# Performance work log

Measured on AMD Instinct MI355X. Metric: run time of the kernel, lower is better.

The kernel has to match this reference:

```python
import jax, jax.numpy as jnp
import numpy as np

STATE_SIZE = 29
ACTION_SIZE = 3


def setup_inputs() -> dict:
    key = jax.random.key(0)
    ks = jax.random.split(key, 12)

    def row_norm(k, shape, scale=1.0):
        w = jax.random.normal(k, shape, dtype=jnp.float32)
        return w * (scale / jnp.sqrt(jnp.sum(w * w, axis=1, keepdims=True)))

    lrelu_gain = float(np.sqrt(2.0 / (1.0 + 0.01 ** 2)))  # torch calculate_gain('leaky_relu')
    inp = {
        "x": jax.random.normal(ks[0], (1, STATE_SIZE), dtype=jnp.float32),
        "hx": jnp.zeros((1, 128), jnp.float32),
        "cx": jnp.zeros((1, 128), jnp.float32),
        "w1": row_norm(ks[1], (256, STATE_SIZE)) * lrelu_gain,
        "b1": jnp.zeros((256,), jnp.float32),
        "w2": row_norm(ks[2], (256, 256)) * lrelu_gain,
        "b2": jnp.zeros((256,), jnp.float32),
        "w3": row_norm(ks[3], (128, 256)) * lrelu_gain,
        "b3": jnp.zeros((128,), jnp.float32),
        "w4": row_norm(ks[4], (128, 128)) * lrelu_gain,
        "b4": jnp.zeros((128,), jnp.float32),
        "w_ih": jax.random.normal(ks[5], (512, 128), dtype=jnp.float32) * 0.08,
        "b_ih": jnp.zeros((512,), jnp.float32),
        "w_hh": jax.random.normal(ks[6], (512, 128), dtype=jnp.float32) * 0.08,
        "b_hh": jnp.zeros((512,), jnp.float32),
        "w_critic": row_norm(ks[7], (1, 128), 1.0),
        "b_critic": jnp.zeros((1,), jnp.float32),
        "w_actor": row_norm(ks[8], (ACTION_SIZE, 128), 0.01),
        "b_actor": jnp.zeros((ACTION_SIZE,), jnp.float32),
        "w_actor2": row_norm(ks[9], (ACTION_SIZE, 128), 0.01),
        "b_actor2": jnp.zeros((ACTION_SIZE,), jnp.float32),
    }
    return inp


def _lrelu(v):
    return jnp.where(v > 0, v, 0.1 * v)


def reference(x, hx, cx, w1, b1, w2, b2, w3, b3, w4, b4,
              w_ih, b_ih, w_hh, b_hh,
              w_critic, b_critic, w_actor, b_actor, w_actor2, b_actor2):
    h = _lrelu(x @ w1.T + b1)
    h = _lrelu(h @ w2.T + b2)
    h = _lrelu(h @ w3.T + b3)
    h = _lrelu(h @ w4.T + b4)            # [1,128]
    # LSTMCell: gate order i, f, g, o (PyTorch convention)
    gates = h @ w_ih.T + b_ih + hx @ w_hh.T + b_hh  # [1,512]
    i, f, g, o = jnp.split(gates, 4, axis=-1)
    c_new = jax.nn.sigmoid(f) * cx + jax.nn.sigmoid(i) * jnp.tanh(g)
    h_new = jax.nn.sigmoid(o) * jnp.tanh(c_new)      # [1,128]
    value = jnp.squeeze(h_new @ w_critic.T + b_critic)          # scalar
    actor = jax.nn.soft_sign(h_new @ w_actor.T + b_actor)
    actor = jnp.squeeze(actor)                                   # [action_size]
    actor2 = jnp.squeeze(h_new @ w_actor2.T + b_actor2)         # [action_size]
    return (value, actor, actor2)
```

## Files before the change

kernel.cpp:

```cpp
#include <hip/hip_runtime.h>
#include <math.h>


#define NB   61
#define TPB  256
#define MAGIC 0x3A3C5A17u

#define H1_OFF 0
#define H2_OFF 256
#define H3_OFF 512
#define PT_OFF 640

__device__ __forceinline__ float lrelu(float v) { return v > 0.f ? v : 0.1f * v; }
__device__ __forceinline__ float sigm(float v)  { return 1.f / (1.f + __expf(-v)); }
__device__ __forceinline__ float dot4(float4 a, float4 b) {
    return a.x * b.x + a.y * b.y + a.z * b.z + a.w * b.w;
}

__device__ __forceinline__ void send(unsigned long long* p, float v) {
    unsigned lo = __float_as_uint(v);
    unsigned long long pk = (unsigned long long)lo |
                            ((unsigned long long)(lo ^ MAGIC) << 32);
    __hip_atomic_store(p, pk, __ATOMIC_RELAXED, __HIP_MEMORY_SCOPE_AGENT);
}
__device__ __forceinline__ float recv(unsigned long long* p) {
    unsigned long long pk =
        __hip_atomic_load(p, __ATOMIC_RELAXED, __HIP_MEMORY_SCOPE_AGENT);
    unsigned lo = (unsigned)pk, hi = (unsigned)(pk >> 32);
    if ((lo ^ MAGIC) == hi) return __uint_as_float(lo);
    __builtin_amdgcn_s_sleep(2);
    for (;;) {
        pk = __hip_atomic_load(p, __ATOMIC_RELAXED, __HIP_MEMORY_SCOPE_AGENT);
        lo = (unsigned)pk; hi = (unsigned)(pk >> 32);
        if ((lo ^ MAGIC) == hi) return __uint_as_float(lo);
        __builtin_amdgcn_s_sleep(8);
    }
}
__device__ __forceinline__ void touch(unsigned long long* p) {
    unsigned long long v =
        __hip_atomic_load(p, __ATOMIC_RELAXED, __HIP_MEMORY_SCOPE_AGENT);
    asm volatile("" :: "v"(v));
}

__global__ __launch_bounds__(TPB, 1) void a3c_fwd(
    const float* __restrict__ x, const float* __restrict__ hx, const float* __restrict__ cx,
    const float* __restrict__ w1, const float* __restrict__ b1,
    const float* __restrict__ w2, const float* __restrict__ b2,
    const float* __restrict__ w3, const float* __restrict__ b3,
    const float* __restrict__ w4, const float* __restrict__ b4,
    const float* __restrict__ w_ih, const float* __restrict__ b_ih,
    const float* __restrict__ w_hh, const float* __restrict__ b_hh,
    const float* __restrict__ w_critic, const float* __restrict__ b_critic,
    const float* __restrict__ w_actor, const float* __restrict__ b_actor,
    const float* __restrict__ w_actor2, const float* __restrict__ b_actor2,
    float* __restrict__ out, unsigned long long* __restrict__ wsp)
{
    const int blk = blockIdx.x, tid = threadIdx.x;

    if (blk < 32) {
        const int g  = blk;
        const int gc = g * 4;
        const int r  = tid >> 4, p = tid & 15;
        const int gate = r >> 2, cell = r & 3;
        const int grow = gate * 128 + gc + cell;
        const int r4 = tid >> 1, p4 = tid & 1;

        if (tid < 8)       touch(wsp + H3_OFF + tid * 16);
        else if (tid == 8) touch(wsp + PT_OFF + g * 8);

        __shared__ __align__(16) float hx_s[128];
        __shared__ __align__(16) float h3_s[128];
        __shared__ __align__(16) float h4_s[128];
        __shared__ __align__(16) float g_s[16];
        __shared__ __align__(16) float hn_s[4];
        __shared__ __align__(16) float hw_s[28];
        __shared__ __align__(16) float hb_s[8];

        float4 ah0, ah1;
        {
            const float4* wp = (const float4*)(w_hh + grow * 128 + p * 8);
            ah0 = wp[0]; ah1 = wp[1];
        }
        float4 a4[16];
        {
            const float4* wp = (const float4*)(w4 + r4 * 128 + p4 * 64);
            #pragma unroll
            for (int j = 0; j < 16; ++j) a4[j] = wp[j];
        }
        float4 ai0, ai1;
        {
            const float4* wp = (const float4*)(w_ih + grow * 128 + p * 8);
            ai0 = wp[0]; ai1 = wp[1];
        }
        const float bsum = b_ih[grow] + b_hh[grow];
        const float bb4  = b4[r4];
        float cxv = (tid < 4) ? cx[gc + tid] : 0.f;

        if (tid < 128) hx_s[tid] = hx[tid];
        if (tid < 28) {
            int o = tid >> 2, c = tid & 3;
            float v;
            if (o == 0)      v = w_critic[gc + c];
            else if (o < 4)  v = w_actor [(o - 1) * 128 + gc + c];
            else             v = w_actor2[(o - 4) * 128 + gc + c];
            hw_s[tid] = v;
        }
        if (g == 0 && tid == 0) {
            hb_s[0] = b_critic[0];
            hb_s[1] = b_actor[0];  hb_s[2] = b_actor[1];  hb_s[3] = b_actor[2];
            hb_s[4] = b_actor2[0]; hb_s[5] = b_actor2[1]; hb_s[6] = b_actor2[2];
        }
        __syncthreads();

        float g0;
        {
            const float4* hp = (const float4*)(hx_s + p * 8);
            float s = dot4(ah0, hp[0]) + dot4(ah1, hp[1]);
            s += __shfl_xor(s, 1); s += __shfl_xor(s, 2);
            s += __shfl_xor(s, 4); s += __shfl_xor(s, 8);
            g0 = s + bsum;
        }

        if (tid < 128) h3_s[tid] = recv(wsp + H3_OFF + tid);
        __syncthreads();

        {
            const float4* hp = (const float4*)(h3_s + p4 * 64);
            float s = 0.f;
            #pragma unroll
            for (int j = 0; j < 16; ++j) s += dot4(a4[j], hp[j]);
            s += __shfl_xor(s, 1);
            if (p4 == 0) h4_s[r4] = lrelu(s + bb4);
        }
        __syncthreads();

        {
            const float4* hp = (const float4*)(h4_s + p * 8);
            float s = dot4(ai0, hp[0]) + dot4(ai1, hp[1]);
            s += __shfl_xor(s, 1); s += __shfl_xor(s, 2);
            s += __shfl_xor(s, 4); s += __shfl_xor(s, 8);
            if (p == 0) g_s[r] = g0 + s;
        }
        __syncthreads();

        if (tid < 4) {
            float ig = g_s[tid];
            float fg = g_s[4 + tid];
            float gg = g_s[8 + tid];
            float og = g_s[12 + tid];
            float c  = sigm(fg) * cxv + sigm(ig) * tanhf(gg);
            hn_s[tid] = sigm(og) * tanhf(c);
        }
        __syncthreads();

        if (tid < 7) {
            const float* wc = hw_s + tid * 4;
            float s = wc[0] * hn_s[0] + wc[1] * hn_s[1]
                    + wc[2] * hn_s[2] + wc[3] * hn_s[3];
            if (g == 0) s += hb_s[tid];
            send(wsp + PT_OFF + g * 8 + tid, s);
        }
        return;
    }

    if (blk < 36) {
        const int row = (blk - 32) * 64 + (tid >> 2), sub = tid & 3;
        if (tid < 4) touch(wsp + H1_OFF + (blk - 32) * 64 + tid * 16);

        float a[8];
        #pragma unroll
        for (int j = 0; j < 8; ++j) {
            int c = sub * 8 + j;
            a[j] = (c < 29) ? w1[row * 29 + c] : 0.f;
        }
        const float bb1 = b1[row];

        __shared__ __align__(16) float x_s[32];
        if (tid < 32) x_s[tid] = (tid < 29) ? x[tid] : 0.f;
        __syncthreads();

        const float* xp = x_s + sub * 8;
        float s = 0.f;
        #pragma unroll
        for (int j = 0; j < 8; ++j) s += a[j] * xp[j];
        s += __shfl_xor(s, 1); s += __shfl_xor(s, 2);
        if (sub == 0) send(wsp + H1_OFF + row, lrelu(s + bb1));
        return;
    }

    if (blk < 52) {
        const int b = blk - 36;
        const int row = b * 16 + (tid >> 4), p = tid & 15;
        if (tid < 16)       touch(wsp + H1_OFF + tid * 16);
        else if (tid == 16) touch(wsp + H2_OFF + b * 16);

        float4 a2[4];
        {
            const float4* wp = (const float4*)(w2 + row * 256 + p * 16);
            #pragma unroll
            for (int j = 0; j < 4; ++j) a2[j] = wp[j];
        }
        const float bb2 = b2[row];

        __shared__ __align__(16) float h1_s[256];
        h1_s[tid] = recv(wsp + H1_OFF + tid);
        __syncthreads();

        const float4* hp = (const float4*)(h1_s + p * 16);
        float s = 0.f;
        #pragma unroll
        for (int j = 0; j < 4; ++j) s += dot4(a2[j], hp[j]);
        s += __shfl_xor(s, 1); s += __shfl_xor(s, 2);
        s += __shfl_xor(s, 4); s += __shfl_xor(s, 8);
        if (p == 0) send(wsp + H2_OFF + row, lrelu(s + bb2));
        return;
    }

    if (blk < 60) {
        const int b = blk - 52;
        const int row = b * 16 + (tid >> 4), p = tid & 15;
        if (tid < 16)       touch(wsp + H2_OFF + tid * 16);
        else if (tid == 16) touch(wsp + H3_OFF + b * 16);

        float4 a3[4];
        {
            const float4* wp = (const float4*)(w3 + row * 256 + p * 16);
            #pragma unroll
            for (int j = 0; j < 4; ++j) a3[j] = wp[j];
        }
        const float bb3 = b3[row];

        __shared__ __align__(16) float h2_s[256];
        h2_s[tid] = recv(wsp + H2_OFF + tid);
        __syncthreads();

        const float4* hp = (const float4*)(h2_s + p * 16);
        float s = 0.f;
        #pragma unroll
        for (int j = 0; j < 4; ++j) s += dot4(a3[j], hp[j]);
        s += __shfl_xor(s, 1); s += __shfl_xor(s, 2);
        s += __shfl_xor(s, 4); s += __shfl_xor(s, 8);
        if (p == 0) send(wsp + H3_OFF + row, lrelu(s + bb3));
        return;
    }

    {
        if (tid < 32) touch(wsp + PT_OFF + tid * 8);
        __shared__ __align__(16) float ps[224];
        const int g = tid >> 3, h = tid & 7;
        if (h < 7) ps[h * 32 + g] = recv(wsp + PT_OFF + g * 8 + h);
        __syncthreads();
        if (tid < 7) {
            const float* row = ps + tid * 32;
            float s = 0.f;
            #pragma unroll
            for (int j = 0; j < 32; ++j) s += row[j];
            if (tid >= 1 && tid <= 3) s = s / (1.f + fabsf(s));
            out[tid] = s;
        }
    }
}

extern "C" void kernel_launch(void* const* d_in, const int* in_sizes, int n_in,
                              void* d_out, int out_size, void* d_ws, size_t ws_size,
                              hipStream_t stream) {
    const float* x        = (const float*)d_in[0];
    const float* hx       = (const float*)d_in[1];
    const float* cx       = (const float*)d_in[2];
    const float* w1       = (const float*)d_in[3];
    const float* b1       = (const float*)d_in[4];
    const float* w2       = (const float*)d_in[5];
    const float* b2       = (const float*)d_in[6];
    const float* w3       = (const float*)d_in[7];
    const float* b3       = (const float*)d_in[8];
    const float* w4       = (const float*)d_in[9];
    const float* b4       = (const float*)d_in[10];
    const float* w_ih     = (const float*)d_in[11];
    const float* b_ih     = (const float*)d_in[12];
    const float* w_hh     = (const float*)d_in[13];
    const float* b_hh     = (const float*)d_in[14];
    const float* w_critic = (const float*)d_in[15];
    const float* b_critic = (const float*)d_in[16];
    const float* w_actor  = (const float*)d_in[17];
    const float* b_actor  = (const float*)d_in[18];
    const float* w_actor2 = (const float*)d_in[19];
    const float* b_actor2 = (const float*)d_in[20];
    float* out = (float*)d_out;
    unsigned long long* wsp = (unsigned long long*)d_ws;

    a3c_fwd<<<NB, TPB, 0, stream>>>(x, hx, cx, w1, b1, w2, b2, w3, b3, w4, b4,
                                    w_ih, b_ih, w_hh, b_hh,
                                    w_critic, b_critic, w_actor, b_actor,
                                    w_actor2, b_actor2, out, wsp);
}
```

Baseline: 103.0 us.

## Re-partition fused MLP+LSTM stages across 41 blocks with fewer cross-block handoffs

Layer 1 is now computed redundantly inside each layer-2 block, which removes the separate layer-1 stage and its global handoff. Layer 4 moves out of the LSTM blocks into its own 4-block stage. The LSTM gate work shrinks to 16 blocks of 8 cells each, and the final reduction sums 16 partials instead of 32. The aim is to cut the number of spin-wait handoffs and total blocks on the serial critical path, at the price of duplicated layer-1 work, more register pressure, and an extra stage boundary between layer 4 and the LSTM.

New measurement: 102.9 us. No clear change (-0.1%).

```diff
diff --git a/kernel.cpp b/kernel.cpp
--- a/kernel.cpp
+++ b/kernel.cpp
@@ -2,14 +2,14 @@
 #include <math.h>
 
 
-#define NB   61
+#define NB   41
 #define TPB  256
 #define MAGIC 0x3A3C5A17u
 
-#define H1_OFF 0
-#define H2_OFF 256
-#define H3_OFF 512
-#define PT_OFF 640
+#define H2_OFF 0
+#define H3_OFF 256
+#define H4_OFF 384
+#define PT_OFF 512
 
 __device__ __forceinline__ float lrelu(float v) { return v > 0.f ? v : 0.1f * v; }
 __device__ __forceinline__ float sigm(float v)  { return 1.f / (1.f + __expf(-v)); }
@@ -57,52 +57,145 @@
 {
     const int blk = blockIdx.x, tid = threadIdx.x;
 
-    if (blk < 32) {
-        const int g  = blk;
-        const int gc = g * 4;
-        const int r  = tid >> 4, p = tid & 15;
-        const int gate = r >> 2, cell = r & 3;
-        const int grow = gate * 128 + gc + cell;
-        const int r4 = tid >> 1, p4 = tid & 1;
-
-        if (tid < 8)       touch(wsp + H3_OFF + tid * 16);
+    if (blk < 16) {
+        const int b = blk;
+        if (tid == 0) touch(wsp + H2_OFF + b * 16);
+        if (tid == 1) touch(wsp + H2_OFF + b * 16 + 8);
+
+        float a1[29];
+        {
+            const float* w1r = w1 + tid * 29;
+            #pragma unroll
+            for (int j = 0; j < 29; ++j) a1[j] = w1r[j];
+        }
+        const float bb1 = b1[tid];
+
+        const int r2 = b * 16 + (tid >> 4), p2 = tid & 15;
+        float4 a2[4];
+        {
+            const float4* wp = (const float4*)(w2 + r2 * 256 + p2 * 16);
+            #pragma unroll
+            for (int j = 0; j < 4; ++j) a2[j] = wp[j];
+        }
+        const float bb2 = b2[r2];
+
+        __shared__ __align__(16) float x_s[32];
+        __shared__ __align__(16) float h1_s[256];
+        if (tid < 32) x_s[tid] = (tid < 29) ? x[tid] : 0.f;
+        __syncthreads();
+
+        {
+            float s = 0.f;
+            #pragma unroll
+            for (int j = 0; j < 29; ++j) s += a1[j] * x_s[j];
+            h1_s[tid] = lrelu(s + bb1);
+        }
+        __syncthreads();
+
+        {
+            const float4* hp = (const float4*)(h1_s + p2 * 16);
+            float s = 0.f;
+            #pragma unroll
+            for (int j = 0; j < 4; ++j) s += dot4(a2[j], hp[j]);
+            s += __shfl_xor(s, 1); s += __shfl_xor(s, 2);
+            s += __shfl_xor(s, 4); s += __shfl_xor(s, 8);
+            if (p2 == 0) send(wsp + H2_OFF + r2, lrelu(s + bb2));
+        }
+        return;
+    }
+
+    if (blk < 20) {
+        const int c = blk - 16;
+        if (tid < 16)       touch(wsp + H2_OFF + tid * 16);
+        else if (tid < 20)  touch(wsp + H3_OFF + c * 32 + (tid - 16) * 8);
+
+        const int r3 = c * 32 + (tid >> 3), p3 = tid & 7;
+        float4 a3[8];
+        {
+            const float4* wp = (const float4*)(w3 + r3 * 256 + p3 * 32);
+            #pragma unroll
+            for (int j = 0; j < 8; ++j) a3[j] = wp[j];
+        }
+        const float bb3 = b3[r3];
+
+        __shared__ __align__(16) float h2_s[256];
+        h2_s[tid] = recv(wsp + H2_OFF + tid);
+        __syncthreads();
+
+        const float4* hp = (const float4*)(h2_s + p3 * 32);
+        float s = 0.f;
+        #pragma unroll
+        for (int j = 0; j < 8; ++j) s += dot4(a3[j], hp[j]);
+        s += __shfl_xor(s, 1); s += __shfl_xor(s, 2); s += __shfl_xor(s, 4);
+        if (p3 == 0) send(wsp + H3_OFF + r3, lrelu(s + bb3));
+        return;
+    }
+
+    if (blk < 24) {
+        const int d = blk - 20;
+        if (tid < 8)        touch(wsp + H3_OFF + tid * 16);
+        else if (tid < 12)  touch(wsp + H4_OFF + d * 32 + (tid - 8) * 8);
+
+        const int r4 = d * 32 + (tid >> 3), p4 = tid & 7;
+        float4 a4[4];
+        {
+            const float4* wp = (const float4*)(w4 + r4 * 128 + p4 * 16);
+            #pragma unroll
+            for (int j = 0; j < 4; ++j) a4[j] = wp[j];
+        }
+        const float bb4 = b4[r4];
+
+        __shared__ __align__(16) float h3_s[128];
+        if (tid < 128) h3_s[tid] = recv(wsp + H3_OFF + tid);
+        __syncthreads();
+
+        const float4* hp = (const float4*)(h3_s + p4 * 16);
+        float s = 0.f;
+        #pragma unroll
+        for (int j = 0; j < 4; ++j) s += dot4(a4[j], hp[j]);
+        s += __shfl_xor(s, 1); s += __shfl_xor(s, 2); s += __shfl_xor(s, 4);
+        if (p4 == 0) send(wsp + H4_OFF + r4, lrelu(s + bb4));
+        return;
+    }
+
+    if (blk < 40) {
+        const int g = blk - 24;
+        if (tid < 8)       touch(wsp + H4_OFF + tid * 16);
         else if (tid == 8) touch(wsp + PT_OFF + g * 8);
 
+        const int r = tid >> 3, p = tid & 7;
+        const int gate = r >> 3, cell = r & 7;
+        const int grow = gate * 128 + g * 8 + cell;
+
+        float4 ah[4];
+        {
+            const float4* wp = (const float4*)(w_hh + grow * 128 + p * 16);
+            #pragma unroll
+            for (int j = 0; j < 4; ++j) ah[j] = wp[j];
+        }
+        float4 ai[4];
+        {
+            const float4* wp = (const float4*)(w_ih + grow * 128 + p * 16);
+            #pragma unroll
+            for (int j = 0; j < 4; ++j) ai[j] = wp[j];
+        }
+        const float bsum = b_ih[grow] + b_hh[grow];
+
         __shared__ __align__(16) float hx_s[128];
-        __shared__ __align__(16) float h3_s[128];
         __shared__ __align__(16) float h4_s[128];
-        __shared__ __align__(16) float g_s[16];
-        __shared__ __align__(16) float hn_s[4];
-        __shared__ __align__(16) float hw_s[28];
+        __shared__ __align__(16) float g_s[32];
+        __shared__ __align__(16) float hn_s[8];
+        __shared__ __align__(16) float hw_s[56];
         __shared__ __align__(16) float hb_s[8];
 
-        float4 ah0, ah1;
-        {
-            const float4* wp = (const float4*)(w_hh + grow * 128 + p * 8);
-            ah0 = wp[0]; ah1 = wp[1];
-        }
-        float4 a4[16];
-        {
-            const float4* wp = (const float4*)(w4 + r4 * 128 + p4 * 64);
-            #pragma unroll
-            for (int j = 0; j < 16; ++j) a4[j] = wp[j];
-        }
-        float4 ai0, ai1;
-        {
-            const float4* wp = (const float4*)(w_ih + grow * 128 + p * 8);
-            ai0 = wp[0]; ai1 = wp[1];
-        }
-        const float bsum = b_ih[grow] + b_hh[grow];
-        const float bb4  = b4[r4];
-        float cxv = (tid < 4) ? cx[gc + tid] : 0.f;
-
         if (tid < 128) hx_s[tid] = hx[tid];
-        if (tid < 28) {
-            int o = tid >> 2, c = tid & 3;
+        float cxv = (tid < 8) ? cx[g * 8 + tid] : 0.f;
+        if (tid < 56) {
+            int o = tid >> 3, c = tid & 7;
             float v;
-            if (o == 0)      v = w_critic[gc + c];
-            else if (o < 4)  v = w_actor [(o - 1) * 128 + gc + c];
-            else             v = w_actor2[(o - 4) * 128 + gc + c];
+            if (o == 0)      v = w_critic[g * 8 + c];
+            else if (o < 4)  v = w_actor [(o - 1) * 128 + g * 8 + c];
+            else             v = w_actor2[(o - 4) * 128 + g * 8 + c];
             hw_s[tid] = v;
         }
         if (g == 0 && tid == 0) {
@@ -114,147 +207,59 @@
 
         float g0;
         {
-            const float4* hp = (const float4*)(hx_s + p * 8);
-            float s = dot4(ah0, hp[0]) + dot4(ah1, hp[1]);
-            s += __shfl_xor(s, 1); s += __shfl_xor(s, 2);
-            s += __shfl_xor(s, 4); s += __shfl_xor(s, 8);
+            const float4* hp = (const float4*)(hx_s + p * 16);
+            float s = 0.f;
+            #pragma unroll
+            for (int j = 0; j < 4; ++j) s += dot4(ah[j], hp[j]);
+            s += __shfl_xor(s, 1); s += __shfl_xor(s, 2); s += __shfl_xor(s, 4);
             g0 = s + bsum;
         }
 
-        if (tid < 128) h3_s[tid] = recv(wsp + H3_OFF + tid);
-        __syncthreads();
-
-        {
-            const float4* hp = (const float4*)(h3_s + p4 * 64);
-            float s = 0.f;
-            #pragma unroll
-            for (int j = 0; j < 16; ++j) s += dot4(a4[j], hp[j]);
-            s += __shfl_xor(s, 1);
-            if (p4 == 0) h4_s[r4] = lrelu(s + bb4);
-        }
-        __syncthreads();
-
-        {
-            const float4* hp = (const float4*)(h4_s + p * 8);
-            float s = dot4(ai0, hp[0]) + dot4(ai1, hp[1]);
-            s += __shfl_xor(s, 1); s += __shfl_xor(s, 2);
-            s += __shfl_xor(s, 4); s += __shfl_xor(s, 8);
+        if (tid < 128) h4_s[tid] = recv(wsp + H4_OFF + tid);
+        __syncthreads();
+
+        {
+            const float4* hp = (const float4*)(h4_s + p * 16);
+            float s = 0.f;
+            #pragma unroll
+            for (int j = 0; j < 4; ++j) s += dot4(ai[j], hp[j]);
+            s += __shfl_xor(s, 1); s += __shfl_xor(s, 2); s += __shfl_xor(s, 4);
             if (p == 0) g_s[r] = g0 + s;
         }
         __syncthreads();
 
-        if (tid < 4) {
+        if (tid < 8) {
             float ig = g_s[tid];
-            float fg = g_s[4 + tid];
-            float gg = g_s[8 + tid];
-            float og = g_s[12 + tid];
+            float fg = g_s[8 + tid];
+            float gg = g_s[16 + tid];
+            float og = g_s[24 + tid];
             float c  = sigm(fg) * cxv + sigm(ig) * tanhf(gg);
             hn_s[tid] = sigm(og) * tanhf(c);
         }
         __syncthreads();
 
         if (tid < 7) {
-            const float* wc = hw_s + tid * 4;
-            float s = wc[0] * hn_s[0] + wc[1] * hn_s[1]
-                    + wc[2] * hn_s[2] + wc[3] * hn_s[3];
+            const float* wc = hw_s + tid * 8;
+            float s = 0.f;
+            #pragma unroll
+            for (int j = 0; j < 8; ++j) s += wc[j] * hn_s[j];
             if (g == 0) s += hb_s[tid];
             send(wsp + PT_OFF + g * 8 + tid, s);
         }
         return;
     }
 
-    if (blk < 36) {
-        const int row = (blk - 32) * 64 + (tid >> 2), sub = tid & 3;
-        if (tid < 4) touch(wsp + H1_OFF + (blk - 32) * 64 + tid * 16);
-
-        float a[8];
-        #pragma unroll
-        for (int j = 0; j < 8; ++j) {
-            int c = sub * 8 + j;
-            a[j] = (c < 29) ? w1[row * 29 + c] : 0.f;
-        }
-        const float bb1 = b1[row];
-
-        __shared__ __align__(16) float x_s[32];
-        if (tid < 32) x_s[tid] = (tid < 29) ? x[tid] : 0.f;
-        __syncthreads();
-
-        const float* xp = x_s + sub * 8;
-        float s = 0.f;
-        #pragma unroll
-        for (int j = 0; j < 8; ++j) s += a[j] * xp[j];
-        s += __shfl_xor(s, 1); s += __shfl_xor(s, 2);
-        if (sub == 0) send(wsp + H1_OFF + row, lrelu(s + bb1));
-        return;
-    }
-
-    if (blk < 52) {
-        const int b = blk - 36;
-        const int row = b * 16 + (tid >> 4), p = tid & 15;
-        if (tid < 16)       touch(wsp + H1_OFF + tid * 16);
-        else if (tid == 16) touch(wsp + H2_OFF + b * 16);
-
-        float4 a2[4];
-        {
-            const float4* wp = (const float4*)(w2 + row * 256 + p * 16);
-            #pragma unroll
-            for (int j = 0; j < 4; ++j) a2[j] = wp[j];
-        }
-        const float bb2 = b2[row];
-
-        __shared__ __align__(16) float h1_s[256];
-        h1_s[tid] = recv(wsp + H1_OFF + tid);
-        __syncthreads();
-
-        const float4* hp = (const float4*)(h1_s + p * 16);
-        float s = 0.f;
-        #pragma unroll
-        for (int j = 0; j < 4; ++j) s += dot4(a2[j], hp[j]);
-        s += __shfl_xor(s, 1); s += __shfl_xor(s, 2);
-        s += __shfl_xor(s, 4); s += __shfl_xor(s, 8);
-        if (p == 0) send(wsp + H2_OFF + row, lrelu(s + bb2));
-        return;
-    }
-
-    if (blk < 60) {
-        const int b = blk - 52;
-        const int row = b * 16 + (tid >> 4), p = tid & 15;
-        if (tid < 16)       touch(wsp + H2_OFF + tid * 16);
-        else if (tid == 16) touch(wsp + H3_OFF + b * 16);
-
-        float4 a3[4];
-        {
-            const float4* wp = (const float4*)(w3 + row * 256 + p * 16);
-            #pragma unroll
-            for (int j = 0; j < 4; ++j) a3[j] = wp[j];
-        }
-        const float bb3 = b3[row];
-
-        __shared__ __align__(16) float h2_s[256];
-        h2_s[tid] = recv(wsp + H2_OFF + tid);
-        __syncthreads();
-
-        const float4* hp = (const float4*)(h2_s + p * 16);
-        float s = 0.f;
-        #pragma unroll
-        for (int j = 0; j < 4; ++j) s += dot4(a3[j], hp[j]);
-        s += __shfl_xor(s, 1); s += __shfl_xor(s, 2);
-        s += __shfl_xor(s, 4); s += __shfl_xor(s, 8);
-        if (p == 0) send(wsp + H3_OFF + row, lrelu(s + bb3));
-        return;
-    }
-
     {
-        if (tid < 32) touch(wsp + PT_OFF + tid * 8);
-        __shared__ __align__(16) float ps[224];
+        if (tid < 16) touch(wsp + PT_OFF + tid * 8);
+        __shared__ __align__(16) float ps[112];
         const int g = tid >> 3, h = tid & 7;
-        if (h < 7) ps[h * 32 + g] = recv(wsp + PT_OFF + g * 8 + h);
+        if (tid < 128 && h < 7) ps[h * 16 + g] = recv(wsp + PT_OFF + g * 8 + h);
         __syncthreads();
         if (tid < 7) {
-            const float* row = ps + tid * 32;
-            float s = 0.f;
-            #pragma unroll
-            for (int j = 0; j < 32; ++j) s += row[j];
+            const float* row = ps + tid * 16;
+            float s = 0.f;
+            #pragma unroll
+            for (int j = 0; j < 16; ++j) s += row[j];
             if (tid >= 1 && tid <= 3) s = s / (1.f + fabsf(s));
             out[tid] = s;
         }
```
